# Kernel optimization log

Measured on AMD Instinct MI355X. Metric: run time of the kernel, lower is better.

The kernel has to match this reference:

```python
import jax, jax.numpy as jnp
import numpy as np

N = 200000   # active voxels
D = 80       # dense grid side
K = 27       # 3x3x3 kernel offsets
CIN, CMID, COUT = 16, 32, 32
EPS = 1e-3   # BatchNorm1d eps from the module


def _build_rulebook():
    """Submanifold conv rulebook: for each kernel offset, (input_idx, output_idx) pairs.
    Padded to length N with dummy output index N (scatter target discarded)."""
    rng = np.random.default_rng(0)
    lin = rng.choice(D ** 3, size=N, replace=False)
    coords = np.stack(np.unravel_index(lin, (D, D, D)), axis=1).astype(np.int64)  # [N,3]
    lookup = np.full(D ** 3, -1, np.int64)
    lookup[lin] = np.arange(N)
    rule_in = np.zeros((K, N), np.int32)
    rule_out = np.full((K, N), N, np.int32)  # dummy row N = padding
    k = 0
    for dx in (-1, 0, 1):
        for dy in (-1, 0, 1):
            for dz in (-1, 0, 1):
                nb = coords + np.array([dx, dy, dz])
                valid = np.all((nb >= 0) & (nb < D), axis=1)
                nb_lin = (nb[valid, 0] * D + nb[valid, 1]) * D + nb[valid, 2]
                idx = lookup[nb_lin]
                hit = idx >= 0
                src = idx[hit].astype(np.int32)
                dst = np.nonzero(valid)[0][hit].astype(np.int32)
                m = src.shape[0]
                rule_in[k, :m] = src
                rule_out[k, :m] = dst
                k += 1
    return rule_in, rule_out


def setup_inputs() -> dict:
    key = jax.random.key(0)
    ks = jax.random.split(key, 3)
    ri, ro = _build_rulebook()
    return {
        "feats": jax.random.normal(ks[0], (N, CIN), jnp.float32),
        "W1": jax.random.normal(ks[1], (K, CIN, CMID), jnp.float32) * 0.05,
        "gamma1": jnp.ones((CMID,), jnp.float32),
        "beta1": jnp.zeros((CMID,), jnp.float32),
        "W2": jax.random.normal(ks[2], (K, CMID, COUT), jnp.float32) * 0.05,
        "gamma2": jnp.ones((COUT,), jnp.float32),
        "beta2": jnp.zeros((COUT,), jnp.float32),
        "rule_in": jnp.asarray(ri),
        "rule_out": jnp.asarray(ro),
    }


def _subm_conv(feats, W, rule_in, rule_out):
    """Gather-GEMM-scatter over kernel offsets (lax.scan keeps one offset resident)."""
    n = feats.shape[0]

    def step(acc, xs):
        in_i, out_i, Wk = xs
        return acc.at[out_i].add(feats[in_i] @ Wk), None

    acc0 = jnp.zeros((n + 1, W.shape[-1]), feats.dtype)  # row n is padding sink
    acc, _ = jax.lax.scan(step, acc0, (rule_in, rule_out, W))
    return acc[:n]


def _bn_relu(x, gamma, beta):
    # BatchNorm1d training-mode forward (biased var) + ReLU
    mu = x.mean(0)
    var = jnp.mean((x - mu) ** 2, 0)
    return jax.nn.relu((x - mu) * jax.lax.rsqrt(var + EPS) * gamma + beta)


def reference(feats, W1, gamma1, beta1, W2, gamma2, beta2, rule_in, rule_out):
    x = _bn_relu(_subm_conv(feats, W1, rule_in, rule_out), gamma1, beta1)
    x = _bn_relu(_subm_conv(x, W2, rule_in, rule_out), gamma2, beta2)
    return x
```

## Files before the change

kernel.cpp:

```cpp
#include <hip/hip_runtime.h>

#define NVOX 200000
#define KOFF 27
#define CIN 16
#define CMID 32
#define COUT 32
#define EPSBN 1e-3f
#define NPAIR 14

typedef _Float16 f16x8 __attribute__((ext_vector_type(8)));
typedef _Float16 f16x4 __attribute__((ext_vector_type(4)));
typedef float f32x4 __attribute__((ext_vector_type(4)));

#define OFF_X1H 21600000
#define OFF_FH  34400064
#define OFF_WB1 40800096
#define OFF_WB2 40828768
#define OFF_ST  40884064

__global__ __launch_bounds__(256) void k_init(const float* __restrict__ feats,
                                              int* __restrict__ gatherT,
                                              _Float16* __restrict__ featsh,
                                              _Float16* __restrict__ x1h,
                                              float* __restrict__ stats) {
  int t = blockIdx.x * 256 + threadIdx.x;
  int stride = gridDim.x * 256;
  for (int i = t; i < KOFF * NVOX; i += stride) gatherT[i] = -1;
  for (int i = t; i < NVOX * CIN / 4; i += stride) {
    float4 f = ((const float4*)feats)[i];
    f16x4 h = {(_Float16)f.x, (_Float16)f.y, (_Float16)f.z, (_Float16)f.w};
    ((f16x4*)featsh)[i] = h;
  }
  if (t < 256) stats[t] = 0.f;
  if (t < CMID) x1h[NVOX * CMID + t] = (_Float16)0.f;
  if (t < CIN) featsh[NVOX * CIN + t] = (_Float16)0.f;
}

__global__ __launch_bounds__(256) void k_build(const int* __restrict__ rule_in,
                                               const int* __restrict__ rule_out,
                                               int* __restrict__ gatherT) {
  int e = blockIdx.x * 256 + threadIdx.x;
  if (e >= KOFF * NVOX) return;
  int k = e / NVOX;
  int dst = rule_out[e];
  if (dst < NVOX) gatherT[k * NVOX + dst] = rule_in[e];
}

__global__ __launch_bounds__(256) void k_prepw(const float* __restrict__ W1,
                                               const float* __restrict__ W2,
                                               _Float16* __restrict__ WB1,
                                               _Float16* __restrict__ WB2) {
  int e = blockIdx.x * 256 + threadIdx.x;
  if (e < NPAIR * 1024) {
    int j = e & 7, l = (e >> 3) & 63, f = (e >> 9) & 1, p = e >> 10;
    int kk = ((l >> 4) << 3) + j;
    int n = (f << 4) + (l & 15);
    int k = 2 * p + (kk >> 4);
    int c = kk & 15;
    float v = (k < KOFF) ? W1[(k * CIN + c) * CMID + n] : 0.f;
    WB1[e] = (_Float16)v;
  }
  int e2 = e - NPAIR * 1024;
  if (e2 >= 0 && e2 < KOFF * 1024) {
    int j = e2 & 7, l = (e2 >> 3) & 63, f = (e2 >> 9) & 1, k = e2 >> 10;
    int kk = ((l >> 4) << 3) + j;
    int n = (f << 4) + (l & 15);
    WB2[e2] = (_Float16)W2[(k * CMID + kk) * COUT + n];
  }
}

__global__ __launch_bounds__(1024, 8) void k_conv1m(const _Float16* __restrict__ featsh,
                                                    const int* __restrict__ gatherT,
                                                    const uint4* __restrict__ WB1,
                                                    _Float16* __restrict__ x1h,
                                                    float* __restrict__ gsums) {
  __shared__ uint4 wlds[NPAIR * 128];
  __shared__ float lsum[64];
  int tid = threadIdx.x;
  for (int i = tid; i < NPAIR * 128; i += 1024) wlds[i] = WB1[i];
  if (tid < 64) lsum[tid] = 0.f;
  __syncthreads();

  int lane = tid & 63, wave = tid >> 6;
  int q = lane >> 4, n = lane & 15;
  int rowbase = blockIdx.x * 256 + wave * 16;
  int row = rowbase + n;
  int rowc = (row < NVOX) ? row : (NVOX - 1);
  int kqoff = q >> 1;
  int eoff = (q & 1) * 8;

  f32x4 c0 = {0.f, 0.f, 0.f, 0.f}, c1 = {0.f, 0.f, 0.f, 0.f};

  int kq0 = kqoff;
  int src = gatherT[kq0 * NVOX + rowc];
  unsigned s = ((unsigned)src >= NVOX) ? NVOX : (unsigned)src;
  f16x8 a = *(const f16x8*)(featsh + s * CIN + eoff);

#pragma unroll 1
  for (int p = 0; p < NPAIR; ++p) {
    int pn = (p + 1 < NPAIR) ? (p + 1) : p;
    int kq2 = 2 * pn + kqoff;
    if (kq2 > KOFF - 1) kq2 = KOFF - 1;
    int src2 = gatherT[kq2 * NVOX + rowc];
    unsigned s2 = ((unsigned)src2 >= NVOX) ? NVOX : (unsigned)src2;
    f16x8 a2 = *(const f16x8*)(featsh + s2 * CIN + eoff);
    f16x8 b0 = ((const f16x8*)wlds)[(p * 2 + 0) * 64 + lane];
    f16x8 b1 = ((const f16x8*)wlds)[(p * 2 + 1) * 64 + lane];
    c0 = __builtin_amdgcn_mfma_f32_16x16x32_f16(a, b0, c0, 0, 0, 0);
    c1 = __builtin_amdgcn_mfma_f32_16x16x32_f16(a, b1, c1, 0, 0, 0);
    a = a2;
  }

  float s0 = 0.f, sq0 = 0.f, s1 = 0.f, sq1 = 0.f;
#pragma unroll
  for (int r = 0; r < 4; ++r) {
    int grow = rowbase + q * 4 + r;
    float mk = (grow < NVOX) ? 1.f : 0.f;
    float v0 = c0[r] * mk, v1 = c1[r] * mk;
    s0 += v0; sq0 += v0 * v0; s1 += v1; sq1 += v1 * v1;
    if (grow < NVOX) {
      x1h[grow * CMID + n] = (_Float16)c0[r];
      x1h[grow * CMID + 16 + n] = (_Float16)c1[r];
    }
  }
#pragma unroll
  for (int msk = 16; msk < 64; msk <<= 1) {
    s0 += __shfl_xor(s0, msk, 64); sq0 += __shfl_xor(sq0, msk, 64);
    s1 += __shfl_xor(s1, msk, 64); sq1 += __shfl_xor(sq1, msk, 64);
  }
  if (lane < 16) {
    atomicAdd(&lsum[n], s0);       atomicAdd(&lsum[16 + n], s1);
    atomicAdd(&lsum[32 + n], sq0); atomicAdd(&lsum[48 + n], sq1);
  }
  __syncthreads();
  if (tid < 64) atomicAdd(&gsums[tid], lsum[tid]);
}

__global__ void k_finalize(const float* __restrict__ sums,
                           const float* __restrict__ gamma,
                           const float* __restrict__ beta,
                           float* __restrict__ ss) {
  int o = threadIdx.x;
  if (o < 32) {
    const float inv_n = 1.0f / (float)NVOX;
    float mu = sums[o] * inv_n;
    float var = sums[32 + o] * inv_n - mu * mu;
    float sc = gamma[o] * rsqrtf(var + EPSBN);
    ss[o] = sc;
    ss[32 + o] = beta[o] - mu * sc;
  }
}

__global__ __launch_bounds__(256) void k_bnrelu1h(_Float16* __restrict__ x1h,
                                                  const float* __restrict__ ss) {
  int t = blockIdx.x * 256 + threadIdx.x;
  if (t >= NVOX * CMID / 8) return;
  f16x8* p = (f16x8*)x1h + t;
  int c = (t & 3) * 8;
  f16x8 v = *p;
#pragma unroll
  for (int i = 0; i < 8; ++i) {
    float x = (float)v[i];
    x = fmaf(x, ss[c + i], ss[32 + c + i]);
    v[i] = (_Float16)fmaxf(x, 0.f);
  }
  *p = v;
}

__global__ __launch_bounds__(1024, 8) void k_conv2m(const _Float16* __restrict__ x1h,
                                                    const int* __restrict__ gatherT,
                                                    const uint4* __restrict__ WB2,
                                                    float* __restrict__ out,
                                                    float* __restrict__ gsums) {
  __shared__ uint4 wlds[KOFF * 128];
  __shared__ float lsum[64];
  int tid = threadIdx.x;
  for (int i = tid; i < KOFF * 128; i += 1024) wlds[i] = WB2[i];
  if (tid < 64) lsum[tid] = 0.f;
  __syncthreads();

  int lane = tid & 63, wave = tid >> 6;
  int q = lane >> 4, n = lane & 15;
  int rowbase = blockIdx.x * 256 + wave * 16;
  int row = rowbase + n;
  int rowc = (row < NVOX) ? row : (NVOX - 1);
  int eoff = q * 8;

  f32x4 c0 = {0.f, 0.f, 0.f, 0.f}, c1 = {0.f, 0.f, 0.f, 0.f};

  int src = gatherT[rowc];
  unsigned s = ((unsigned)src >= NVOX) ? NVOX : (unsigned)src;
  f16x8 a = *(const f16x8*)(x1h + s * CMID + eoff);

#pragma unroll 1
  for (int k = 0; k < KOFF; ++k) {
    int kn = (k + 1 < KOFF) ? (k + 1) : k;
    int src2 = gatherT[kn * NVOX + rowc];
    unsigned s2 = ((unsigned)src2 >= NVOX) ? NVOX : (unsigned)src2;
    f16x8 a2 = *(const f16x8*)(x1h + s2 * CMID + eoff);
    f16x8 b0 = ((const f16x8*)wlds)[(k * 2 + 0) * 64 + lane];
    f16x8 b1 = ((const f16x8*)wlds)[(k * 2 + 1) * 64 + lane];
    c0 = __builtin_amdgcn_mfma_f32_16x16x32_f16(a, b0, c0, 0, 0, 0);
    c1 = __builtin_amdgcn_mfma_f32_16x16x32_f16(a, b1, c1, 0, 0, 0);
    a = a2;
  }

  float s0 = 0.f, sq0 = 0.f, s1 = 0.f, sq1 = 0.f;
#pragma unroll
  for (int r = 0; r < 4; ++r) {
    int grow = rowbase + q * 4 + r;
    float mk = (grow < NVOX) ? 1.f : 0.f;
    float v0 = c0[r] * mk, v1 = c1[r] * mk;
    s0 += v0; sq0 += v0 * v0; s1 += v1; sq1 += v1 * v1;
    if (grow < NVOX) {
      out[grow * COUT + n] = c0[r];
      out[grow * COUT + 16 + n] = c1[r];
    }
  }
#pragma unroll
  for (int msk = 16; msk < 64; msk <<= 1) {
    s0 += __shfl_xor(s0, msk, 64); sq0 += __shfl_xor(sq0, msk, 64);
    s1 += __shfl_xor(s1, msk, 64); sq1 += __shfl_xor(sq1, msk, 64);
  }
  if (lane < 16) {
    atomicAdd(&lsum[n], s0);       atomicAdd(&lsum[16 + n], s1);
    atomicAdd(&lsum[32 + n], sq0); atomicAdd(&lsum[48 + n], sq1);
  }
  __syncthreads();
  if (tid < 64) atomicAdd(&gsums[tid], lsum[tid]);
}

__global__ __launch_bounds__(256) void k_bnrelu2(float* __restrict__ out,
                                                 const float* __restrict__ ss) {
  int t = blockIdx.x * 256 + threadIdx.x;
  if (t >= NVOX * COUT / 4) return;
  float4* p = (float4*)out + t;
  int c = (t & 7) * 4;
  float4 v = *p;
  v.x = fmaxf(fmaf(v.x, ss[c + 0], ss[32 + c + 0]), 0.f);
  v.y = fmaxf(fmaf(v.y, ss[c + 1], ss[32 + c + 1]), 0.f);
  v.z = fmaxf(fmaf(v.z, ss[c + 2], ss[32 + c + 2]), 0.f);
  v.w = fmaxf(fmaf(v.w, ss[c + 3], ss[32 + c + 3]), 0.f);
  *p = v;
}

extern "C" void kernel_launch(void* const* d_in, const int* in_sizes, int n_in,
                              void* d_out, int out_size, void* d_ws, size_t ws_size,
                              hipStream_t stream) {
  const float* feats  = (const float*)d_in[0];
  const float* W1     = (const float*)d_in[1];
  const float* gamma1 = (const float*)d_in[2];
  const float* beta1  = (const float*)d_in[3];
  const float* W2     = (const float*)d_in[4];
  const float* gamma2 = (const float*)d_in[5];
  const float* beta2  = (const float*)d_in[6];
  const int* rule_in  = (const int*)d_in[7];
  const int* rule_out = (const int*)d_in[8];
  float* out = (float*)d_out;

  int*       gatherT = (int*)d_ws;
  _Float16*  x1h     = (_Float16*)((char*)d_ws + OFF_X1H);
  _Float16*  featsh  = (_Float16*)((char*)d_ws + OFF_FH);
  _Float16*  WB1     = (_Float16*)((char*)d_ws + OFF_WB1);
  _Float16*  WB2     = (_Float16*)((char*)d_ws + OFF_WB2);
  float*     stats   = (float*)((char*)d_ws + OFF_ST);

  k_init<<<2048, 256, 0, stream>>>(feats, gatherT, featsh, x1h, stats);
  k_build<<<(KOFF * NVOX + 255) / 256, 256, 0, stream>>>(rule_in, rule_out, gatherT);
  k_prepw<<<164, 256, 0, stream>>>(W1, W2, WB1, WB2);
  k_conv1m<<<782, 1024, 0, stream>>>(featsh, gatherT, (const uint4*)WB1, x1h, stats);
  k_finalize<<<1, 64, 0, stream>>>(stats, gamma1, beta1, stats + 64);
  k_bnrelu1h<<<(NVOX * CMID / 8 + 255) / 256, 256, 0, stream>>>(x1h, stats + 64);
  k_conv2m<<<782, 1024, 0, stream>>>(x1h, gatherT, (const uint4*)WB2, out, stats + 128);
  k_finalize<<<1, 64, 0, stream>>>(stats + 128, gamma2, beta2, stats + 192);
  k_bnrelu2<<<(NVOX * COUT / 4 + 255) / 256, 256, 0, stream>>>(out, stats + 192);
}
```

Before: 227.7 us.

## Switch convs to 32x32x16 MFMA, merge prep kernels, fold BN finalize into apply

Both conv kernels move from paired 16x16x32 MFMAs to the 32x32x16 MFMA with 32 rows per wave and 512-thread blocks. All 27 gather indices are prefetched into registers and the offset loop is fully unrolled, so gathers can be issued early. Init, rulebook build and weight prep are merged into one kernel, with hipMemsetAsync doing the fills, and the BN finalize step is recomputed inside each apply kernel. This cuts launches and should raise MFMA efficiency and memory parallelism, at the cost of more registers per thread and redundant finalize work in every thread.

```diff
diff --git a/kernel.cpp b/kernel.cpp
--- a/kernel.cpp
+++ b/kernel.cpp
@@ -6,241 +6,212 @@
 #define CMID 32
 #define COUT 32
 #define EPSBN 1e-3f
-#define NPAIR 14
 
 typedef _Float16 f16x8 __attribute__((ext_vector_type(8)));
 typedef _Float16 f16x4 __attribute__((ext_vector_type(4)));
-typedef float f32x4 __attribute__((ext_vector_type(4)));
+typedef float f32x16 __attribute__((ext_vector_type(16)));
 
 #define OFF_X1H 21600000
 #define OFF_FH  34400064
 #define OFF_WB1 40800096
-#define OFF_WB2 40828768
-#define OFF_ST  40884064
-
-__global__ __launch_bounds__(256) void k_init(const float* __restrict__ feats,
-                                              int* __restrict__ gatherT,
-                                              _Float16* __restrict__ featsh,
-                                              _Float16* __restrict__ x1h,
-                                              float* __restrict__ stats) {
-  int t = blockIdx.x * 256 + threadIdx.x;
-  int stride = gridDim.x * 256;
-  for (int i = t; i < KOFF * NVOX; i += stride) gatherT[i] = -1;
-  for (int i = t; i < NVOX * CIN / 4; i += stride) {
-    float4 f = ((const float4*)feats)[i];
-    f16x4 h = {(_Float16)f.x, (_Float16)f.y, (_Float16)f.z, (_Float16)f.w};
-    ((f16x4*)featsh)[i] = h;
-  }
-  if (t < 256) stats[t] = 0.f;
-  if (t < CMID) x1h[NVOX * CMID + t] = (_Float16)0.f;
-  if (t < CIN) featsh[NVOX * CIN + t] = (_Float16)0.f;
-}
+#define OFF_WB2 40827744
+#define OFF_ST  40883040
 
 __global__ __launch_bounds__(256) void k_build(const int* __restrict__ rule_in,
                                                const int* __restrict__ rule_out,
-                                               int* __restrict__ gatherT) {
+                                               const float* __restrict__ feats,
+                                               const float* __restrict__ W1,
+                                               const float* __restrict__ W2,
+                                               int* __restrict__ gatherT,
+                                               _Float16* __restrict__ featsh,
+                                               _Float16* __restrict__ WB1,
+                                               _Float16* __restrict__ WB2,
+                                               _Float16* __restrict__ x1h) {
   int e = blockIdx.x * 256 + threadIdx.x;
-  if (e >= KOFF * NVOX) return;
-  int k = e / NVOX;
-  int dst = rule_out[e];
-  if (dst < NVOX) gatherT[k * NVOX + dst] = rule_in[e];
-}
-
-__global__ __launch_bounds__(256) void k_prepw(const float* __restrict__ W1,
-                                               const float* __restrict__ W2,
-                                               _Float16* __restrict__ WB1,
-                                               _Float16* __restrict__ WB2) {
-  int e = blockIdx.x * 256 + threadIdx.x;
-  if (e < NPAIR * 1024) {
-    int j = e & 7, l = (e >> 3) & 63, f = (e >> 9) & 1, p = e >> 10;
-    int kk = ((l >> 4) << 3) + j;
-    int n = (f << 4) + (l & 15);
-    int k = 2 * p + (kk >> 4);
-    int c = kk & 15;
-    float v = (k < KOFF) ? W1[(k * CIN + c) * CMID + n] : 0.f;
-    WB1[e] = (_Float16)v;
-  }
-  int e2 = e - NPAIR * 1024;
-  if (e2 >= 0 && e2 < KOFF * 1024) {
-    int j = e2 & 7, l = (e2 >> 3) & 63, f = (e2 >> 9) & 1, k = e2 >> 10;
-    int kk = ((l >> 4) << 3) + j;
-    int n = (f << 4) + (l & 15);
-    WB2[e2] = (_Float16)W2[(k * CMID + kk) * COUT + n];
-  }
-}
-
-__global__ __launch_bounds__(1024, 8) void k_conv1m(const _Float16* __restrict__ featsh,
-                                                    const int* __restrict__ gatherT,
-                                                    const uint4* __restrict__ WB1,
-                                                    _Float16* __restrict__ x1h,
-                                                    float* __restrict__ gsums) {
-  __shared__ uint4 wlds[NPAIR * 128];
+  if (e < KOFF * NVOX) {
+    int k = e / NVOX;
+    int dst = rule_out[e];
+    if (dst < NVOX) gatherT[k * NVOX + dst] = rule_in[e];
+  }
+  if (e < NVOX * CIN / 4) {
+    float4 f = ((const float4*)feats)[e];
+    f16x4 h = {(_Float16)f.x, (_Float16)f.y, (_Float16)f.z, (_Float16)f.w};
+    ((f16x4*)featsh)[e] = h;
+  }
+  if (e < KOFF * 512) {
+    int j = e & 7, l = (e >> 3) & 63, k = e >> 9;
+    int kk = ((l >> 5) << 3) + j;
+    int n = l & 31;
+    WB1[e] = (_Float16)W1[(k * CIN + kk) * CMID + n];
+  }
+  if (e < KOFF * 1024) {
+    int j = e & 7, l = (e >> 3) & 63, f = (e >> 9) & 1, k = e >> 10;
+    int kk = (f << 4) + ((l >> 5) << 3) + j;
+    int n = l & 31;
+    WB2[e] = (_Float16)W2[(k * CMID + kk) * COUT + n];
+  }
+  if (e < CMID) x1h[(size_t)NVOX * CMID + e] = (_Float16)0.f;
+  if (e < CIN) featsh[(size_t)NVOX * CIN + e] = (_Float16)0.f;
+}
+
+__global__ __launch_bounds__(512, 4) void k_conv1m(const _Float16* __restrict__ featsh,
+                                                   const int* __restrict__ gatherT,
+                                                   const uint4* __restrict__ WB1,
+                                                   _Float16* __restrict__ x1h,
+                                                   float* __restrict__ gsums) {
+  __shared__ uint4 wlds[KOFF * 64];
   __shared__ float lsum[64];
   int tid = threadIdx.x;
-  for (int i = tid; i < NPAIR * 128; i += 1024) wlds[i] = WB1[i];
+  for (int i = tid; i < KOFF * 64; i += 512) wlds[i] = WB1[i];
   if (tid < 64) lsum[tid] = 0.f;
   __syncthreads();
 
   int lane = tid & 63, wave = tid >> 6;
-  int q = lane >> 4, n = lane & 15;
-  int rowbase = blockIdx.x * 256 + wave * 16;
-  int row = rowbase + n;
+  int m = lane & 31, khalf = lane >> 5;
+  int rowbase = blockIdx.x * 256 + wave * 32;
+  int row = rowbase + m;
   int rowc = (row < NVOX) ? row : (NVOX - 1);
-  int kqoff = q >> 1;
-  int eoff = (q & 1) * 8;
-
-  f32x4 c0 = {0.f, 0.f, 0.f, 0.f}, c1 = {0.f, 0.f, 0.f, 0.f};
-
-  int kq0 = kqoff;
-  int src = gatherT[kq0 * NVOX + rowc];
-  unsigned s = ((unsigned)src >= NVOX) ? NVOX : (unsigned)src;
-  f16x8 a = *(const f16x8*)(featsh + s * CIN + eoff);
-
-#pragma unroll 1
-  for (int p = 0; p < NPAIR; ++p) {
-    int pn = (p + 1 < NPAIR) ? (p + 1) : p;
-    int kq2 = 2 * pn + kqoff;
-    if (kq2 > KOFF - 1) kq2 = KOFF - 1;
-    int src2 = gatherT[kq2 * NVOX + rowc];
-    unsigned s2 = ((unsigned)src2 >= NVOX) ? NVOX : (unsigned)src2;
-    f16x8 a2 = *(const f16x8*)(featsh + s2 * CIN + eoff);
-    f16x8 b0 = ((const f16x8*)wlds)[(p * 2 + 0) * 64 + lane];
-    f16x8 b1 = ((const f16x8*)wlds)[(p * 2 + 1) * 64 + lane];
-    c0 = __builtin_amdgcn_mfma_f32_16x16x32_f16(a, b0, c0, 0, 0, 0);
-    c1 = __builtin_amdgcn_mfma_f32_16x16x32_f16(a, b1, c1, 0, 0, 0);
-    a = a2;
-  }
-
-  float s0 = 0.f, sq0 = 0.f, s1 = 0.f, sq1 = 0.f;
-#pragma unroll
-  for (int r = 0; r < 4; ++r) {
-    int grow = rowbase + q * 4 + r;
+
+  int idx[KOFF];
+#pragma unroll
+  for (int k = 0; k < KOFF; ++k) idx[k] = gatherT[k * NVOX + rowc];
+
+  f32x16 c;
+#pragma unroll
+  for (int i = 0; i < 16; ++i) c[i] = 0.f;
+
+#pragma unroll
+  for (int k = 0; k < KOFF; ++k) {
+    unsigned s = ((unsigned)idx[k] < (unsigned)NVOX) ? (unsigned)idx[k] : (unsigned)NVOX;
+    f16x8 a = *(const f16x8*)(featsh + (size_t)s * CIN + (khalf << 3));
+    f16x8 b = ((const f16x8*)wlds)[k * 64 + lane];
+    c = __builtin_amdgcn_mfma_f32_32x32x16_f16(a, b, c, 0, 0, 0);
+  }
+
+  float s0 = 0.f, q0 = 0.f;
+#pragma unroll
+  for (int r = 0; r < 16; ++r) {
+    int grow = rowbase + (r & 3) + ((r >> 2) << 3) + (khalf << 2);
     float mk = (grow < NVOX) ? 1.f : 0.f;
-    float v0 = c0[r] * mk, v1 = c1[r] * mk;
-    s0 += v0; sq0 += v0 * v0; s1 += v1; sq1 += v1 * v1;
-    if (grow < NVOX) {
-      x1h[grow * CMID + n] = (_Float16)c0[r];
-      x1h[grow * CMID + 16 + n] = (_Float16)c1[r];
-    }
-  }
-#pragma unroll
-  for (int msk = 16; msk < 64; msk <<= 1) {
-    s0 += __shfl_xor(s0, msk, 64); sq0 += __shfl_xor(sq0, msk, 64);
-    s1 += __shfl_xor(s1, msk, 64); sq1 += __shfl_xor(sq1, msk, 64);
-  }
-  if (lane < 16) {
-    atomicAdd(&lsum[n], s0);       atomicAdd(&lsum[16 + n], s1);
-    atomicAdd(&lsum[32 + n], sq0); atomicAdd(&lsum[48 + n], sq1);
+    float v = c[r] * mk;
+    s0 += v; q0 += v * v;
+    if (grow < NVOX) x1h[(size_t)grow * CMID + m] = (_Float16)c[r];
+  }
+  s0 += __shfl_xor(s0, 32, 64);
+  q0 += __shfl_xor(q0, 32, 64);
+  if (lane < 32) {
+    atomicAdd(&lsum[m], s0);
+    atomicAdd(&lsum[32 + m], q0);
   }
   __syncthreads();
   if (tid < 64) atomicAdd(&gsums[tid], lsum[tid]);
 }
 
-__global__ void k_finalize(const float* __restrict__ sums,
-                           const float* __restrict__ gamma,
-                           const float* __restrict__ beta,
-                           float* __restrict__ ss) {
-  int o = threadIdx.x;
-  if (o < 32) {
-    const float inv_n = 1.0f / (float)NVOX;
-    float mu = sums[o] * inv_n;
-    float var = sums[32 + o] * inv_n - mu * mu;
-    float sc = gamma[o] * rsqrtf(var + EPSBN);
-    ss[o] = sc;
-    ss[32 + o] = beta[o] - mu * sc;
-  }
-}
-
 __global__ __launch_bounds__(256) void k_bnrelu1h(_Float16* __restrict__ x1h,
-                                                  const float* __restrict__ ss) {
+                                                  const float* __restrict__ sums,
+                                                  const float* __restrict__ gamma,
+                                                  const float* __restrict__ beta) {
   int t = blockIdx.x * 256 + threadIdx.x;
   if (t >= NVOX * CMID / 8) return;
+  int c = (t & 3) * 8;
+  const float inv_n = 1.0f / (float)NVOX;
+  float sc[8], sh[8];
+#pragma unroll
+  for (int i = 0; i < 8; ++i) {
+    float mu = sums[c + i] * inv_n;
+    float var = sums[32 + c + i] * inv_n - mu * mu;
+    float s = gamma[c + i] * rsqrtf(var + EPSBN);
+    sc[i] = s; sh[i] = beta[c + i] - mu * s;
+  }
   f16x8* p = (f16x8*)x1h + t;
-  int c = (t & 3) * 8;
   f16x8 v = *p;
 #pragma unroll
   for (int i = 0; i < 8; ++i) {
-    float x = (float)v[i];
-    x = fmaf(x, ss[c + i], ss[32 + c + i]);
+    float x = fmaf((float)v[i], sc[i], sh[i]);
     v[i] = (_Float16)fmaxf(x, 0.f);
   }
   *p = v;
 }
 
-__global__ __launch_bounds__(1024, 8) void k_conv2m(const _Float16* __restrict__ x1h,
-                                                    const int* __restrict__ gatherT,
-                                                    const uint4* __restrict__ WB2,
-                                                    float* __restrict__ out,
-                                                    float* __restrict__ gsums) {
+__global__ __launch_bounds__(512, 4) void k_conv2m(const _Float16* __restrict__ x1h,
+                                                   const int* __restrict__ gatherT,
+                                                   const uint4* __restrict__ WB2,
+                                                   float* __restrict__ out,
+                                                   float* __restrict__ gsums) {
   __shared__ uint4 wlds[KOFF * 128];
   __shared__ float lsum[64];
   int tid = threadIdx.x;
-  for (int i = tid; i < KOFF * 128; i += 1024) wlds[i] = WB2[i];
+  for (int i = tid; i < KOFF * 128; i += 512) wlds[i] = WB2[i];
   if (tid < 64) lsum[tid] = 0.f;
   __syncthreads();
 
   int lane = tid & 63, wave = tid >> 6;
-  int q = lane >> 4, n = lane & 15;
-  int rowbase = blockIdx.x * 256 + wave * 16;
-  int row = rowbase + n;
+  int m = lane & 31, khalf = lane >> 5;
+  int rowbase = blockIdx.x * 256 + wave * 32;
+  int row = rowbase + m;
   int rowc = (row < NVOX) ? row : (NVOX - 1);
-  int eoff = q * 8;
-
-  f32x4 c0 = {0.f, 0.f, 0.f, 0.f}, c1 = {0.f, 0.f, 0.f, 0.f};
-
-  int src = gatherT[rowc];
-  unsigned s = ((unsigned)src >= NVOX) ? NVOX : (unsigned)src;
-  f16x8 a = *(const f16x8*)(x1h + s * CMID + eoff);
-
-#pragma unroll 1
+
+  int idx[KOFF];
+#pragma unroll
+  for (int k = 0; k < KOFF; ++k) idx[k] = gatherT[k * NVOX + rowc];
+
+  f32x16 c;
+#pragma unroll
+  for (int i = 0; i < 16; ++i) c[i] = 0.f;
+
+#pragma unroll
   for (int k = 0; k < KOFF; ++k) {
-    int kn = (k + 1 < KOFF) ? (k + 1) : k;
-    int src2 = gatherT[kn * NVOX + rowc];
-    unsigned s2 = ((unsigned)src2 >= NVOX) ? NVOX : (unsigned)src2;
-    f16x8 a2 = *(const f16x8*)(x1h + s2 * CMID + eoff);
+    unsigned s = ((unsigned)idx[k] < (unsigned)NVOX) ? (unsigned)idx[k] : (unsigned)NVOX;
+    const _Float16* rp = x1h + (size_t)s * CMID + (khalf << 3);
+    f16x8 a0 = *(const f16x8*)(rp);
+    f16x8 a1 = *(const f16x8*)(rp + 16);
     f16x8 b0 = ((const f16x8*)wlds)[(k * 2 + 0) * 64 + lane];
     f16x8 b1 = ((const f16x8*)wlds)[(k * 2 + 1) * 64 + lane];
-    c0 = __builtin_amdgcn_mfma_f32_16x16x32_f16(a, b0, c0, 0, 0, 0);
-    c1 = __builtin_amdgcn_mfma_f32_16x16x32_f16(a, b1, c1, 0, 0, 0);
-    a = a2;
-  }
-
-  float s0 = 0.f, sq0 = 0.f, s1 = 0.f, sq1 = 0.f;
-#pragma unroll
-  for (int r = 0; r < 4; ++r) {
-    int grow = rowbase + q * 4 + r;
+    c = __builtin_amdgcn_mfma_f32_32x32x16_f16(a0, b0, c, 0, 0, 0);
+    c = __builtin_amdgcn_mfma_f32_32x32x16_f16(a1, b1, c, 0, 0, 0);
+  }
+
+  float s0 = 0.f, q0 = 0.f;
+#pragma unroll
+  for (int r = 0; r < 16; ++r) {
+    int grow = rowbase + (r & 3) + ((r >> 2) << 3) + (khalf << 2);
     float mk = (grow < NVOX) ? 1.f : 0.f;
-    float v0 = c0[r] * mk, v1 = c1[r] * mk;
-    s0 += v0; sq0 += v0 * v0; s1 += v1; sq1 += v1 * v1;
-    if (grow < NVOX) {
-      out[grow * COUT + n] = c0[r];
-      out[grow * COUT + 16 + n] = c1[r];
-    }
-  }
-#pragma unroll
-  for (int msk = 16; msk < 64; msk <<= 1) {
-    s0 += __shfl_xor(s0, msk, 64); sq0 += __shfl_xor(sq0, msk, 64);
-    s1 += __shfl_xor(s1, msk, 64); sq1 += __shfl_xor(sq1, msk, 64);
-  }
-  if (lane < 16) {
-    atomicAdd(&lsum[n], s0);       atomicAdd(&lsum[16 + n], s1);
-    atomicAdd(&lsum[32 + n], sq0); atomicAdd(&lsum[48 + n], sq1);
+    float v = c[r] * mk;
+    s0 += v; q0 += v * v;
+    if (grow < NVOX) out[(size_t)grow * COUT + m] = c[r];
+  }
+  s0 += __shfl_xor(s0, 32, 64);
+  q0 += __shfl_xor(q0, 32, 64);
+  if (lane < 32) {
+    atomicAdd(&lsum[m], s0);
+    atomicAdd(&lsum[32 + m], q0);
   }
   __syncthreads();
   if (tid < 64) atomicAdd(&gsums[tid], lsum[tid]);
 }
 
 __global__ __launch_bounds__(256) void k_bnrelu2(float* __restrict__ out,
-                                                 const float* __restrict__ ss) {
+                                                 const float* __restrict__ sums,
+                                                 const float* __restrict__ gamma,
+                                                 const float* __restrict__ beta) {
   int t = blockIdx.x * 256 + threadIdx.x;
   if (t >= NVOX * COUT / 4) return;
+  int c = (t & 7) * 4;
+  const float inv_n = 1.0f / (float)NVOX;
+  float sc[4], sh[4];
+#pragma unroll
+  for (int i = 0; i < 4; ++i) {
+    float mu = sums[c + i] * inv_n;
+    float var = sums[32 + c + i] * inv_n - mu * mu;
+    float s = gamma[c + i] * rsqrtf(var + EPSBN);
+    sc[i] = s; sh[i] = beta[c + i] - mu * s;
+  }
   float4* p = (float4*)out + t;
-  int c = (t & 7) * 4;
   float4 v = *p;
-  v.x = fmaxf(fmaf(v.x, ss[c + 0], ss[32 + c + 0]), 0.f);
-  v.y = fmaxf(fmaf(v.y, ss[c + 1], ss[32 + c + 1]), 0.f);
-  v.z = fmaxf(fmaf(v.z, ss[c + 2], ss[32 + c + 2]), 0.f);
-  v.w = fmaxf(fmaf(v.w, ss[c + 3], ss[32 + c + 3]), 0.f);
+  v.x = fmaxf(fmaf(v.x, sc[0], sh[0]), 0.f);
+  v.y = fmaxf(fmaf(v.y, sc[1], sh[1]), 0.f);
+  v.z = fmaxf(fmaf(v.z, sc[2], sh[2]), 0.f);
+  v.w = fmaxf(fmaf(v.w, sc[3], sh[3]), 0.f);
   *p = v;
 }
 
@@ -265,13 +236,12 @@
   _Float16*  WB2     = (_Float16*)((char*)d_ws + OFF_WB2);
   float*     stats   = (float*)((char*)d_ws + OFF_ST);
 
-  k_init<<<2048, 256, 0, stream>>>(feats, gatherT, featsh, x1h, stats);
-  k_build<<<(KOFF * NVOX + 255) / 256, 256, 0, stream>>>(rule_in, rule_out, gatherT);
-  k_prepw<<<164, 256, 0, stream>>>(W1, W2, WB1, WB2);
-  k_conv1m<<<782, 1024, 0, stream>>>(featsh, gatherT, (const uint4*)WB1, x1h, stats);
-  k_finalize<<<1, 64, 0, stream>>>(stats, gamma1, beta1, stats + 64);
-  k_bnrelu1h<<<(NVOX * CMID / 8 + 255) / 256, 256, 0, stream>>>(x1h, stats + 64);
-  k_conv2m<<<782, 1024, 0, stream>>>(x1h, gatherT, (const uint4*)WB2, out, stats + 128);
-  k_finalize<<<1, 64, 0, stream>>>(stats + 128, gamma2, beta2, stats + 192);
-  k_bnrelu2<<<(NVOX * COUT / 4 + 255) / 256, 256, 0, stream>>>(out, stats + 192);
-}
+  hipMemsetAsync(gatherT, 0xFF, (size_t)KOFF * NVOX * 4, stream);
+  hipMemsetAsync(stats, 0, 128 * 4, stream);
+  k_build<<<(KOFF * NVOX + 255) / 256, 256, 0, stream>>>(
+      rule_in, rule_out, feats, W1, W2, gatherT, featsh, WB1, WB2, x1h);
+  k_conv1m<<<782, 512, 0, stream>>>(featsh, gatherT, (const uint4*)WB1, x1h, stats);
+  k_bnrelu1h<<<(NVOX * CMID / 8 + 255) / 256, 256, 0, stream>>>(x1h, stats, gamma1, beta1);
+  k_conv2m<<<782, 512, 0, stream>>>(x1h, gatherT, (const uint4*)WB2, out, stats + 64);
+  k_bnrelu2<<<(NVOX * COUT / 4 + 255) / 256, 256, 0, stream>>>(out, stats + 64, gamma2, beta2);
+}
```

Measured after the change: 217.3 us. -4.6%, faster.
